# Performance work log

Hardware: AMD Instinct MI355X
Metric: run time of the kernel (lower is better)

Reference implementation:

```python
import jax, jax.numpy as jnp
import numpy as np

INPUT_SIZE = 512
HIDDEN = 1024
NUM_CLASSES = 1000
BATCH = 64
SEQ = 512


def setup_inputs() -> dict:
    key = jax.random.key(0)
    ks = jax.random.split(key, 12)
    comb = INPUT_SIZE + HIDDEN
    s = 1.0 / np.sqrt(comb)
    sf = 1.0 / np.sqrt(HIDDEN)
    return {
        "x": jax.random.normal(ks[0], (BATCH, SEQ, INPUT_SIZE), dtype=jnp.float32),
        "Wz_w": jax.random.uniform(ks[1], (HIDDEN, comb), jnp.float32, -s, s),
        "Wz_b": jax.random.uniform(ks[2], (HIDDEN,), jnp.float32, -s, s),
        "Wr_w": jax.random.uniform(ks[3], (HIDDEN, comb), jnp.float32, -s, s),
        "Wr_b": jax.random.uniform(ks[4], (HIDDEN,), jnp.float32, -s, s),
        "Wc_w": jax.random.uniform(ks[5], (HIDDEN, comb), jnp.float32, -s, s),
        "Wc_b": jax.random.uniform(ks[6], (HIDDEN,), jnp.float32, -s, s),
        "Wo_w": jax.random.uniform(ks[7], (HIDDEN, comb), jnp.float32, -s, s),
        "Wo_b": jax.random.uniform(ks[8], (HIDDEN,), jnp.float32, -s, s),
        "fc_w": jax.random.uniform(ks[9], (NUM_CLASSES, HIDDEN), jnp.float32, -sf, sf),
        "fc_b": jax.random.uniform(ks[10], (NUM_CLASSES,), jnp.float32, -sf, sf),
    }


def reference(x, Wz_w, Wz_b, Wr_w, Wr_b, Wc_w, Wc_b, Wo_w, Wo_b, fc_w, fc_b):
    B, T, _ = x.shape
    H = Wz_w.shape[0]

    def step(carry, x_t):
        h, c = carry
        combined = jnp.concatenate([x_t, h], axis=1)          # [B, I+H]
        z = jax.nn.sigmoid(combined @ Wz_w.T + Wz_b)
        r = jax.nn.sigmoid(combined @ Wr_w.T + Wr_b)
        combined_reset = jnp.concatenate([x_t, r * c], axis=1)
        c_tilde = jnp.tanh(combined_reset @ Wc_w.T + Wc_b)
        c_new = z * c + (1.0 - z) * c_tilde
        o = jax.nn.sigmoid(combined @ Wo_w.T + Wo_b)
        h_new = o * jnp.tanh(c_new)
        return (h_new, c_new), None

    h0 = jnp.zeros((B, H), dtype=x.dtype)
    c0 = jnp.zeros((B, H), dtype=x.dtype)
    xs = jnp.swapaxes(x, 0, 1)                                # [T, B, I]
    (h, c), _ = jax.lax.scan(step, (h0, c0), xs)
    # dropout is identity (p=0 / eval mode)
    return h @ fc_w.T + fc_b                                  # [B, num_classes]
```

## Files before the change

### kernel.cpp

```cpp
#include <hip/hip_runtime.h>

#define NWG 128
#define TSTEPS 512

typedef __attribute__((ext_vector_type(8))) short short8;
typedef __attribute__((ext_vector_type(4))) float f32x4;
typedef __attribute__((ext_vector_type(4))) int int4v;

#define T0_OFF   0
#define T1_OFF   49152
#define T2_OFF   98304
#define ZBUF_OFF 135168
#define OBUF_OFF 137248
#define XCB_OFF  139328
#define CST_OFF  141408
#define RCS_OFF  143488
#define HST_OFF  145568
#define BIAS_OFF 147648
#define LDS_BYTES 147776
#define PAD 65

__device__ inline unsigned short f2bf(float f) {
  unsigned int b = __float_as_uint(f);
  return (unsigned short)((b + 0x7FFFu + ((b >> 16) & 1u)) >> 16);
}
__device__ inline float sigm(float x) { return 1.f / (1.f + __expf(-x)); }
__device__ inline float tanh_f(float x) { float e = __expf(2.f * x); return 1.f - 2.f / (e + 1.f); }

__device__ inline short8 cvt8(f32x4 a, f32x4 b) {
  int w0, w1, w2, w3;
  asm("v_cvt_pk_bf16_f32 %0, %1, %2" : "=v"(w0) : "v"(a[0]), "v"(a[1]));
  asm("v_cvt_pk_bf16_f32 %0, %1, %2" : "=v"(w1) : "v"(a[2]), "v"(a[3]));
  asm("v_cvt_pk_bf16_f32 %0, %1, %2" : "=v"(w2) : "v"(b[0]), "v"(b[1]));
  asm("v_cvt_pk_bf16_f32 %0, %1, %2" : "=v"(w3) : "v"(b[2]), "v"(b[3]));
  int4v r = {w0, w1, w2, w3};
  return __builtin_bit_cast(short8, r);
}

__device__ inline void cstore16(void* p, short8 v) {
  asm volatile("global_store_dwordx4 %0, %1, off sc0 sc1" :: "v"(p), "v"(v) : "memory");
}
__device__ inline void cstore4(void* p, int v) {
  asm volatile("global_store_dword %0, %1, off sc0 sc1" :: "v"(p), "v"(v) : "memory");
}
__device__ inline int cload4(const void* p) {
  int v;
  asm volatile("global_load_dword %0, %1, off sc0 sc1\n\ts_waitcnt vmcnt(0)"
               : "=&v"(v) : "v"(p) : "memory");
  return v;
}
__device__ inline void vmdrain() {
  asm volatile("s_waitcnt vmcnt(0)" ::: "memory");
}
__device__ inline void vmwait16() {
  asm volatile("s_waitcnt vmcnt(16)" ::: "memory");
}

__device__ inline void cload16_issue(const unsigned short* p, short8* a) {
  asm volatile(
    "global_load_dwordx4 %0,  %16, off sc0 sc1\n\t"
    "global_load_dwordx4 %1,  %16, off offset:64 sc0 sc1\n\t"
    "global_load_dwordx4 %2,  %16, off offset:128 sc0 sc1\n\t"
    "global_load_dwordx4 %3,  %16, off offset:192 sc0 sc1\n\t"
    "global_load_dwordx4 %4,  %16, off offset:256 sc0 sc1\n\t"
    "global_load_dwordx4 %5,  %16, off offset:320 sc0 sc1\n\t"
    "global_load_dwordx4 %6,  %16, off offset:384 sc0 sc1\n\t"
    "global_load_dwordx4 %7,  %16, off offset:448 sc0 sc1\n\t"
    "global_load_dwordx4 %8,  %16, off offset:512 sc0 sc1\n\t"
    "global_load_dwordx4 %9,  %16, off offset:576 sc0 sc1\n\t"
    "global_load_dwordx4 %10, %16, off offset:640 sc0 sc1\n\t"
    "global_load_dwordx4 %11, %16, off offset:704 sc0 sc1\n\t"
    "global_load_dwordx4 %12, %16, off offset:768 sc0 sc1\n\t"
    "global_load_dwordx4 %13, %16, off offset:832 sc0 sc1\n\t"
    "global_load_dwordx4 %14, %16, off offset:896 sc0 sc1\n\t"
    "global_load_dwordx4 %15, %16, off offset:960 sc0 sc1"
    : "=&v"(a[0]), "=&v"(a[1]), "=&v"(a[2]), "=&v"(a[3]),
      "=&v"(a[4]), "=&v"(a[5]), "=&v"(a[6]), "=&v"(a[7]),
      "=&v"(a[8]), "=&v"(a[9]), "=&v"(a[10]), "=&v"(a[11]),
      "=&v"(a[12]), "=&v"(a[13]), "=&v"(a[14]), "=&v"(a[15])
    : "v"(p)
    : "memory");
}

__device__ inline void gload16_issue_s128(const float* p, f32x4* a) {
  asm volatile(
    "global_load_dwordx4 %0,  %16, off\n\t"
    "global_load_dwordx4 %1,  %16, off offset:128\n\t"
    "global_load_dwordx4 %2,  %16, off offset:256\n\t"
    "global_load_dwordx4 %3,  %16, off offset:384\n\t"
    "global_load_dwordx4 %4,  %16, off offset:512\n\t"
    "global_load_dwordx4 %5,  %16, off offset:640\n\t"
    "global_load_dwordx4 %6,  %16, off offset:768\n\t"
    "global_load_dwordx4 %7,  %16, off offset:896\n\t"
    "global_load_dwordx4 %8,  %16, off offset:1024\n\t"
    "global_load_dwordx4 %9,  %16, off offset:1152\n\t"
    "global_load_dwordx4 %10, %16, off offset:1280\n\t"
    "global_load_dwordx4 %11, %16, off offset:1408\n\t"
    "global_load_dwordx4 %12, %16, off offset:1536\n\t"
    "global_load_dwordx4 %13, %16, off offset:1664\n\t"
    "global_load_dwordx4 %14, %16, off offset:1792\n\t"
    "global_load_dwordx4 %15, %16, off offset:1920"
    : "=&v"(a[0]), "=&v"(a[1]), "=&v"(a[2]), "=&v"(a[3]),
      "=&v"(a[4]), "=&v"(a[5]), "=&v"(a[6]), "=&v"(a[7]),
      "=&v"(a[8]), "=&v"(a[9]), "=&v"(a[10]), "=&v"(a[11]),
      "=&v"(a[12]), "=&v"(a[13]), "=&v"(a[14]), "=&v"(a[15])
    : "v"(p)
    : "memory");
}

__global__ void __launch_bounds__(256, 1) lmgru_kernel(
    const float* __restrict__ x,
    const float* __restrict__ Wz, const float* __restrict__ bz,
    const float* __restrict__ Wr, const float* __restrict__ br,
    const float* __restrict__ Wc, const float* __restrict__ bc,
    const float* __restrict__ Wo, const float* __restrict__ bo,
    const float* __restrict__ fcw, const float* __restrict__ fcb,
    float* __restrict__ out, char* __restrict__ ws)
{
  extern __shared__ char lds[];
  const int tid  = threadIdx.x;
  const int wg   = blockIdx.x;
  const int lane = tid & 63;
  const int q    = tid >> 6;

  unsigned short* hbuf  = (unsigned short*)ws;
  unsigned short* rcbuf = (unsigned short*)(ws + 262144);
  float*          h32   = (float*)(ws + 655360);
  int* hflag  = (int*)(ws + 524288);
  int* rcflag = hflag + 2048;

  float* zbuf = (float*)(lds + ZBUF_OFF);
  float* obuf = (float*)(lds + OBUF_OFF);
  float* xcb  = (float*)(lds + XCB_OFF);
  float* cst  = (float*)(lds + CST_OFF);
  float* rcs  = (float*)(lds + RCS_OFF);
  float* hst  = (float*)(lds + HST_OFF);
  float* bias = (float*)(lds + BIAS_OFF);

  const float* Wg[4] = {Wz, Wr, Wo, Wc};

  for (int it = 0; it < 12; ++it) {
    int slot = tid + 256 * it;
    int s = slot >> 6, l = slot & 63;
    int nn = l & 15, kg = (l >> 4) & 3;
    int k = 32 * s + kg * 8;
    int g = (nn < 8) ? 0 : 1;
    const float* src = Wg[g] + (8 * wg + (nn & 7)) * 1536 + k;
    short8 pk;
    #pragma unroll
    for (int j = 0; j < 8; ++j) pk[j] = (short)f2bf(src[j]);
    *(short8*)(lds + T0_OFF + s * 1024 + l * 16) = pk;
  }
  for (int it = 0; it < 12; ++it) {
    int slot = tid + 256 * it;
    int s = slot >> 6, l = slot & 63;
    int nn = l & 15, kg = (l >> 4) & 3;
    int k = 32 * s + kg * 8;
    int g = (nn < 8) ? 2 : 3;
    short8 pk = {};
    if (g == 2 || k < 512) {
      const float* src = Wg[g] + (8 * wg + (nn & 7)) * 1536 + k;
      #pragma unroll
      for (int j = 0; j < 8; ++j) pk[j] = (short)f2bf(src[j]);
    }
    *(short8*)(lds + T1_OFF + s * 1024 + l * 16) = pk;
  }
  for (int it = 0; it < 8; ++it) {
    int slot = tid + 256 * it;
    int s = slot >> 6, l = slot & 63;
    int nn = l & 15, kg = (l >> 4) & 3;
    int k = 32 * s + kg * 8;
    short8 pk = {};
    if (nn < 8) {
      const float* src = Wc + (8 * wg + nn) * 1536 + 512 + k;
      #pragma unroll
      for (int j = 0; j < 8; ++j) pk[j] = (short)f2bf(src[j]);
    }
    *(short8*)(lds + T2_OFF + s * 1024 + l * 16) = pk;
  }
  if (tid < 32) {
    const float* Bg[4] = {bz, br, bo, bc};
    bias[tid] = Bg[tid >> 3][8 * wg + (tid & 7)];
  }
  for (int i2 = tid; i2 < 8 * PAD; i2 += 256) cst[i2] = 0.f;
  if (tid < 64) {
    short8 z8 = {};
    cstore16(hbuf + tid * 1024 + 8 * wg, z8);
  }
  __syncthreads();
  if (tid == 0) {
    vmdrain();
    cstore4(hflag + wg * 16, 0);
    cstore4(rcflag + wg * 16, 0);
  }

  const int nn  = lane & 15;
  const int kg8 = ((lane >> 4) & 3) * 8;
  const int rbase = ((lane >> 4) & 3) * 4;
  const int brow  = 16 * q + nn;
  const f32x4 zero4 = {0.f, 0.f, 0.f, 0.f};

  for (int t = 1; t <= TSTEPS; ++t) {
    const int pc = t & 1, pp = (t - 1) & 1;

    f32x4 xa[16], xb[16];
    {
      const float* xp = x + brow * 262144 + (t - 1) * 512 + kg8;
      gload16_issue_s128(xp, xa);
      gload16_issue_s128(xp + 4, xb);
    }
    if (tid < 128) {
      const int* fp = hflag + tid * 16;
      while (cload4(fp) < t - 1) __builtin_amdgcn_s_sleep(1);
    }
    __syncthreads();
    vmdrain();
    __builtin_amdgcn_sched_barrier(0);
    short8 axf[16];
    #pragma unroll
    for (int j = 0; j < 16; ++j) axf[j] = cvt8(xa[j], xb[j]);

    f32x4 acc0a = zero4, acc0b = zero4, acc1a = zero4, acc1b = zero4;
    const unsigned short* hb = hbuf + pp * 65536 + brow * 1024;
    short8 ah0[16], ah1[16];
    cload16_issue(hb + kg8, ah0);
    cload16_issue(hb + 512 + kg8, ah1);
    #pragma unroll
    for (int j = 0; j < 16; ++j) {
      short8 b0 = *(const short8*)(lds + T0_OFF + j * 1024 + lane * 16);
      short8 b1 = *(const short8*)(lds + T1_OFF + j * 1024 + lane * 16);
      f32x4& A0 = (j & 1) ? acc0b : acc0a;
      f32x4& A1 = (j & 1) ? acc1b : acc1a;
      A0 = __builtin_amdgcn_mfma_f32_16x16x32_bf16(axf[j], b0, A0, 0, 0, 0);
      A1 = __builtin_amdgcn_mfma_f32_16x16x32_bf16(axf[j], b1, A1, 0, 0, 0);
    }
    vmwait16();
    __builtin_amdgcn_sched_barrier(0);
    #pragma unroll
    for (int j = 0; j < 16; ++j) {
      int s = 16 + j;
      short8 b0 = *(const short8*)(lds + T0_OFF + s * 1024 + lane * 16);
      short8 b1 = *(const short8*)(lds + T1_OFF + s * 1024 + lane * 16);
      f32x4& A0 = (j & 1) ? acc0b : acc0a;
      f32x4& A1 = (j & 1) ? acc1b : acc1a;
      A0 = __builtin_amdgcn_mfma_f32_16x16x32_bf16(ah0[j], b0, A0, 0, 0, 0);
      A1 = __builtin_amdgcn_mfma_f32_16x16x32_bf16(ah0[j], b1, A1, 0, 0, 0);
    }
    vmdrain();
    __builtin_amdgcn_sched_barrier(0);
    #pragma unroll
    for (int j = 0; j < 16; ++j) {
      int s = 32 + j;
      short8 b0 = *(const short8*)(lds + T0_OFF + s * 1024 + lane * 16);
      short8 b1 = *(const short8*)(lds + T1_OFF + s * 1024 + lane * 16);
      f32x4& A0 = (j & 1) ? acc0b : acc0a;
      f32x4& A1 = (j & 1) ? acc1b : acc1a;
      A0 = __builtin_amdgcn_mfma_f32_16x16x32_bf16(ah1[j], b0, A0, 0, 0, 0);
      A1 = __builtin_amdgcn_mfma_f32_16x16x32_bf16(ah1[j], b1, A1, 0, 0, 0);
    }
    {
      f32x4 acc0 = acc0a + acc0b, acc1 = acc1a + acc1b;
      #pragma unroll
      for (int i = 0; i < 4; ++i) {
        int b = 16 * q + rbase + i;
        float v0 = acc0[i] + bias[nn];
        float v1 = acc1[i] + bias[16 + nn];
        if (nn < 8) {
          zbuf[nn * PAD + b] = sigm(v0);
          obuf[nn * PAD + b] = sigm(v1);
        } else {
          int u = nn - 8;
          rcs[u * PAD + b] = sigm(v0) * cst[u * PAD + b];
          xcb[u * PAD + b] = v1;
        }
      }
    }
    __syncthreads();
    if (tid < 64) {
      short8 pk;
      #pragma unroll
      for (int u = 0; u < 8; ++u) pk[u] = (short)f2bf(rcs[u * PAD + tid]);
      cstore16(rcbuf + pc * 65536 + tid * 1024 + 8 * wg, pk);
      vmdrain();
      if (tid == 0) cstore4(rcflag + wg * 16, t);
    }

    if (tid < 128) {
      const int* fp = rcflag + tid * 16;
      while (cload4(fp) < t) __builtin_amdgcn_s_sleep(1);
    }
    __syncthreads();

    f32x4 acca = zero4, accb = zero4;
    const unsigned short* rb = rcbuf + pc * 65536 + brow * 1024;
    short8 ar0[16], ar1[16];
    cload16_issue(rb + kg8, ar0);
    cload16_issue(rb + 512 + kg8, ar1);
    vmwait16();
    __builtin_amdgcn_sched_barrier(0);
    #pragma unroll
    for (int j = 0; j < 16; ++j) {
      short8 bf = *(const short8*)(lds + T2_OFF + j * 1024 + lane * 16);
      f32x4& A = (j & 1) ? accb : acca;
      A = __builtin_amdgcn_mfma_f32_16x16x32_bf16(ar0[j], bf, A, 0, 0, 0);
    }
    vmdrain();
    __builtin_amdgcn_sched_barrier(0);
    #pragma unroll
    for (int j = 0; j < 16; ++j) {
      int s = 16 + j;
      short8 bf = *(const short8*)(lds + T2_OFF + s * 1024 + lane * 16);
      f32x4& A = (j & 1) ? accb : acca;
      A = __builtin_amdgcn_mfma_f32_16x16x32_bf16(ar1[j], bf, A, 0, 0, 0);
    }
    if (nn < 8) {
      f32x4 acc = acca + accb;
      #pragma unroll
      for (int i = 0; i < 4; ++i) {
        int b = 16 * q + rbase + i;
        float ct = tanh_f(acc[i] + xcb[nn * PAD + b]);
        float z  = zbuf[nn * PAD + b];
        float cn = z * cst[nn * PAD + b] + (1.f - z) * ct;
        cst[nn * PAD + b] = cn;
        hst[nn * PAD + b] = obuf[nn * PAD + b] * tanh_f(cn);
      }
    }
    __syncthreads();
    if (tid < 64) {
      if (t < TSTEPS) {
        short8 pk;
        #pragma unroll
        for (int u = 0; u < 8; ++u) pk[u] = (short)f2bf(hst[u * PAD + tid]);
        cstore16(hbuf + pc * 65536 + tid * 1024 + 8 * wg, pk);
        vmdrain();
        if (tid == 0) cstore4(hflag + wg * 16, t);
      } else {
        #pragma unroll
        for (int u = 0; u < 8; ++u) h32[tid * 1024 + 8 * wg + u] = hst[u * PAD + tid];
        if (tid == 0)
          __hip_atomic_store(hflag + wg * 16, t, __ATOMIC_RELEASE, __HIP_MEMORY_SCOPE_AGENT);
      }
    }
  }

  if (tid < 128) {
    while (__hip_atomic_load(hflag + tid * 16, __ATOMIC_RELAXED, __HIP_MEMORY_SCOPE_AGENT) < TSTEPS)
      __builtin_amdgcn_s_sleep(1);
  }
  __syncthreads();
  __builtin_amdgcn_fence(__ATOMIC_ACQUIRE, "agent");

  if (wg < 125) {
    for (int cc = 0; cc < 2; ++cc) {
      int c = 8 * wg + 2 * q + cc;
      const float* wrow = fcw + c * 1024;
      for (int b = 0; b < 64; ++b) {
        const float* hrow = h32 + b * 1024;
        float s = 0.f;
        for (int kk = lane; kk < 1024; kk += 64) s = __builtin_fmaf(hrow[kk], wrow[kk], s);
        #pragma unroll
        for (int off = 32; off; off >>= 1) s += __shfl_xor(s, off);
        if (lane == 0) out[b * 1000 + c] = s + fcb[c];
      }
    }
  }
}

extern "C" void kernel_launch(void* const* d_in, const int* in_sizes, int n_in,
                              void* d_out, int out_size, void* d_ws, size_t ws_size,
                              hipStream_t stream) {
  (void)in_sizes; (void)n_in; (void)out_size; (void)ws_size;
  const float* x   = (const float*)d_in[0];
  const float* Wz  = (const float*)d_in[1];
  const float* bz  = (const float*)d_in[2];
  const float* Wr  = (const float*)d_in[3];
  const float* br  = (const float*)d_in[4];
  const float* Wc  = (const float*)d_in[5];
  const float* bc  = (const float*)d_in[6];
  const float* Wo  = (const float*)d_in[7];
  const float* bo  = (const float*)d_in[8];
  const float* fcw = (const float*)d_in[9];
  const float* fcb = (const float*)d_in[10];

  hipFuncSetAttribute((const void*)lmgru_kernel,
                      hipFuncAttributeMaxDynamicSharedMemorySize, LDS_BYTES);

  hipLaunchKernelGGL(lmgru_kernel, dim3(NWG), dim3(256), LDS_BYTES, stream,
                     x, Wz, bz, Wr, br, Wc, bc, Wo, bo, fcw, fcb,
                     (float*)d_out, (char*)d_ws);
}
```

Measured before the change: 8.598 ms.

## Replicate h and r*c exchange buffers per XCD group to localize reads

Each workgroup now writes its slice of the bf16 hidden-state and r*c exchange buffers into R=8 replicas, and each workgroup reads only the replica picked by its index modulo 8. Because workgroups are typically spread round-robin over the MI355X's 8 XCDs, each replica is read from only one XCD, so the reads are meant to hit that XCD's local L2 instead of going through cross-die traffic. The cost is eight times as many coherent stores per step before the flag is published, plus a larger workspace. A fallback to one replica is kept for when the workspace is too small.

```diff
diff --git a/kernel.cpp b/kernel.cpp
--- a/kernel.cpp
+++ b/kernel.cpp
@@ -20,6 +20,8 @@
 #define LDS_BYTES 147776
 #define PAD 65
 
+#define REP_SHORTS 131072
+
 __device__ inline unsigned short f2bf(float f) {
   unsigned int b = __float_as_uint(f);
   return (unsigned short)((b + 0x7FFFu + ((b >> 16) & 1u)) >> 16);
@@ -49,12 +51,8 @@
                : "=&v"(v) : "v"(p) : "memory");
   return v;
 }
-__device__ inline void vmdrain() {
-  asm volatile("s_waitcnt vmcnt(0)" ::: "memory");
-}
-__device__ inline void vmwait16() {
-  asm volatile("s_waitcnt vmcnt(16)" ::: "memory");
-}
+__device__ inline void vmdrain()  { asm volatile("s_waitcnt vmcnt(0)"  ::: "memory"); }
+__device__ inline void vmwait16() { asm volatile("s_waitcnt vmcnt(16)" ::: "memory"); }
 
 __device__ inline void cload16_issue(const unsigned short* p, short8* a) {
   asm volatile(
@@ -108,6 +106,7 @@
     : "memory");
 }
 
+template<int R>
 __global__ void __launch_bounds__(256, 1) lmgru_kernel(
     const float* __restrict__ x,
     const float* __restrict__ Wz, const float* __restrict__ bz,
@@ -123,11 +122,11 @@
   const int lane = tid & 63;
   const int q    = tid >> 6;
 
-  unsigned short* hbuf  = (unsigned short*)ws;
-  unsigned short* rcbuf = (unsigned short*)(ws + 262144);
-  float*          h32   = (float*)(ws + 655360);
-  int* hflag  = (int*)(ws + 524288);
-  int* rcflag = hflag + 2048;
+  unsigned short* hbuf0  = (unsigned short*)ws;
+  unsigned short* rcbuf0 = (unsigned short*)(ws + (size_t)R * 262144);
+  int*   hflag  = (int*)(ws + (size_t)2 * R * 262144);
+  int*   rcflag = hflag + 2048;
+  float* h32    = (float*)(ws + (size_t)2 * R * 262144 + 65536);
 
   float* zbuf = (float*)(lds + ZBUF_OFF);
   float* obuf = (float*)(lds + OBUF_OFF);
@@ -185,7 +184,9 @@
   for (int i2 = tid; i2 < 8 * PAD; i2 += 256) cst[i2] = 0.f;
   if (tid < 64) {
     short8 z8 = {};
-    cstore16(hbuf + tid * 1024 + 8 * wg, z8);
+    #pragma unroll
+    for (int r = 0; r < R; ++r)
+      cstore16(hbuf0 + r * REP_SHORTS + tid * 1024 + 8 * wg, z8);
   }
   __syncthreads();
   if (tid == 0) {
@@ -200,6 +201,9 @@
   const int brow  = 16 * q + nn;
   const f32x4 zero4 = {0.f, 0.f, 0.f, 0.f};
 
+  unsigned short* myh  = hbuf0  + (wg & (R - 1)) * REP_SHORTS;
+  unsigned short* myrc = rcbuf0 + (wg & (R - 1)) * REP_SHORTS;
+
   for (int t = 1; t <= TSTEPS; ++t) {
     const int pc = t & 1, pp = (t - 1) & 1;
 
@@ -221,7 +225,7 @@
     for (int j = 0; j < 16; ++j) axf[j] = cvt8(xa[j], xb[j]);
 
     f32x4 acc0a = zero4, acc0b = zero4, acc1a = zero4, acc1b = zero4;
-    const unsigned short* hb = hbuf + pp * 65536 + brow * 1024;
+    const unsigned short* hb = myh + pp * 65536 + brow * 1024;
     short8 ah0[16], ah1[16];
     cload16_issue(hb + kg8, ah0);
     cload16_issue(hb + 512 + kg8, ah1);
@@ -280,7 +284,9 @@
       short8 pk;
       #pragma unroll
       for (int u = 0; u < 8; ++u) pk[u] = (short)f2bf(rcs[u * PAD + tid]);
-      cstore16(rcbuf + pc * 65536 + tid * 1024 + 8 * wg, pk);
+      #pragma unroll
+      for (int r = 0; r < R; ++r)
+        cstore16(rcbuf0 + r * REP_SHORTS + pc * 65536 + tid * 1024 + 8 * wg, pk);
       vmdrain();
       if (tid == 0) cstore4(rcflag + wg * 16, t);
     }
@@ -292,7 +298,7 @@
     __syncthreads();
 
     f32x4 acca = zero4, accb = zero4;
-    const unsigned short* rb = rcbuf + pc * 65536 + brow * 1024;
+    const unsigned short* rb = myrc + pc * 65536 + brow * 1024;
     short8 ar0[16], ar1[16];
     cload16_issue(rb + kg8, ar0);
     cload16_issue(rb + 512 + kg8, ar1);
@@ -331,7 +337,9 @@
         short8 pk;
         #pragma unroll
         for (int u = 0; u < 8; ++u) pk[u] = (short)f2bf(hst[u * PAD + tid]);
-        cstore16(hbuf + pc * 65536 + tid * 1024 + 8 * wg, pk);
+        #pragma unroll
+        for (int r = 0; r < R; ++r)
+          cstore16(hbuf0 + r * REP_SHORTS + pc * 65536 + tid * 1024 + 8 * wg, pk);
         vmdrain();
         if (tid == 0) cstore4(hflag + wg * 16, t);
       } else {
@@ -348,6 +356,7 @@
       __builtin_amdgcn_s_sleep(1);
   }
   __syncthreads();
+  vmdrain();
   __builtin_amdgcn_fence(__ATOMIC_ACQUIRE, "agent");
 
   if (wg < 125) {
@@ -369,7 +378,7 @@
 extern "C" void kernel_launch(void* const* d_in, const int* in_sizes, int n_in,
                               void* d_out, int out_size, void* d_ws, size_t ws_size,
                               hipStream_t stream) {
-  (void)in_sizes; (void)n_in; (void)out_size; (void)ws_size;
+  (void)in_sizes; (void)n_in; (void)out_size;
   const float* x   = (const float*)d_in[0];
   const float* Wz  = (const float*)d_in[1];
   const float* bz  = (const float*)d_in[2];
@@ -382,10 +391,19 @@
   const float* fcw = (const float*)d_in[9];
   const float* fcb = (const float*)d_in[10];
 
-  hipFuncSetAttribute((const void*)lmgru_kernel,
-                      hipFuncAttributeMaxDynamicSharedMemorySize, LDS_BYTES);
-
-  hipLaunchKernelGGL(lmgru_kernel, dim3(NWG), dim3(256), LDS_BYTES, stream,
-                     x, Wz, bz, Wr, br, Wc, bc, Wo, bo, fcw, fcb,
-                     (float*)d_out, (char*)d_ws);
-}
+  const size_t NEED8 = (size_t)2 * 8 * 262144 + 65536 + 262144;
+
+  if (ws_size >= NEED8) {
+    hipFuncSetAttribute((const void*)lmgru_kernel<8>,
+                        hipFuncAttributeMaxDynamicSharedMemorySize, LDS_BYTES);
+    hipLaunchKernelGGL(lmgru_kernel<8>, dim3(NWG), dim3(256), LDS_BYTES, stream,
+                       x, Wz, bz, Wr, br, Wc, bc, Wo, bo, fcw, fcb,
+                       (float*)d_out, (char*)d_ws);
+  } else {
+    hipFuncSetAttribute((const void*)lmgru_kernel<1>,
+                        hipFuncAttributeMaxDynamicSharedMemorySize, LDS_BYTES);
+    hipLaunchKernelGGL(lmgru_kernel<1>, dim3(NWG), dim3(256), LDS_BYTES, stream,
+                       x, Wz, bz, Wr, br, Wc, bc, Wo, bo, fcw, fcb,
+                       (float*)d_out, (char*)d_ws);
+  }
+}
```

Measured after the change: 9.989 ms. 16.2% more time.
